# Kernel optimization log

Measured on AMD Instinct MI355X. Metric: run time of the kernel, lower is better.

Reference implementation:

```python
import jax, jax.numpy as jnp
import numpy as np

B, T, DIM = 2, 1024, 1024
H, DH, E, K = 8, 64, 5, 3
SCALE = DH ** -0.5


def topk_mask(scores, k):
    # 0/1 mask of the top-k entries along the last (expert) axis
    _, idx = jax.lax.top_k(scores, k)          # [..., k]
    return jax.nn.one_hot(idx, scores.shape[-1], dtype=scores.dtype).sum(-2)


def setup_inputs() -> dict:
    key = jax.random.key(0)
    ks = jax.random.split(key, 7)
    s = DIM ** -0.5
    x = jax.random.normal(ks[0], (B, T, DIM), jnp.float32)
    Wq = jax.random.normal(ks[1], (DIM, H * DH), jnp.float32) * s
    Wk = jax.random.normal(ks[2], (DIM, H * DH), jnp.float32) * s
    Wv = jax.random.normal(ks[3], (DIM, H * E * DH), jnp.float32) * s
    Ws = jax.random.normal(ks[4], (DIM, H * E), jnp.float32) * s
    Wd = jax.random.normal(ks[5], (DIM, H * E), jnp.float32) * s
    # grouped conv weight: per head h, expert e: map dim_head -> dim
    Wo = jax.random.normal(ks[6], (H, E, DIM, DH), jnp.float32) * (DH ** -0.5)
    causal_mask = jnp.triu(jnp.ones((T, T), bool), 1)[None, None]  # [1,1,T,T]
    return {"x": x, "Wq": Wq, "Wk": Wk, "Wv": Wv, "Ws": Ws, "Wd": Wd,
            "Wo": Wo, "causal_mask": causal_mask}


def reference(x, Wq, Wk, Wv, Ws, Wd, Wo, causal_mask):
    # source-side routing scores (soft: gate values kept on top-k)
    ss = jax.nn.sigmoid((x @ Ws).reshape(B, T, H, E))
    ss = ss * topk_mask(ss, K)
    # destination-side routing (hard 0/1 top-k mask)
    sd = topk_mask(jax.nn.sigmoid((x @ Wd).reshape(B, T, H, E)), K)

    q = (x @ Wq).reshape(B, T, H, DH).transpose(0, 2, 1, 3)  # [B,H,T,DH]
    k = (x @ Wk).reshape(B, T, H, DH).transpose(0, 2, 1, 3)
    v_exp = (x @ Wv).reshape(B, T, H, E, DH)                  # per-expert V
    v = jnp.einsum('bthe,bthed->bhtd', ss, v_exp)             # routed V mix

    scores = jnp.einsum('bhid,bhjd->bhij', q * SCALE, k)
    scores = jnp.where(causal_mask, -1e9, scores)
    probs = jax.nn.softmax(scores, axis=-1)
    o = jnp.einsum('bhij,bhjd->bhid', probs, v)               # [B,H,T,DH]

    # expert output projection (h,e: DH -> DIM), gated by sd, summed over h,e
    out = jnp.einsum('bthe,bhtc,hedc->btd', sd, o, Wo)        # [B,T,DIM]
    return out
```

## Files before the change

### kernel.cpp

```cpp
#include <hip/hip_runtime.h>

typedef unsigned short u16;
typedef __bf16 bf16x8 __attribute__((ext_vector_type(8)));
typedef float floatx4 __attribute__((ext_vector_type(4)));

#define B_   2
#define T_   1024
#define DIM_ 1024
#define H_   8
#define DH_  64
#define E_   5

#define N1   3584
#define M_   2048
#define KOUT 2560

__device__ __forceinline__ u16 f2bf(float f) {
  union { float f; unsigned u; } v; v.f = f;
  unsigned r = v.u + 0x7FFFu + ((v.u >> 16) & 1u);
  return (u16)(r >> 16);
}
__device__ __forceinline__ float bf2f(u16 h) {
  union { unsigned u; float f; } v; v.u = ((unsigned)h) << 16;
  return v.f;
}

__device__ __forceinline__ void async_cp16(const void* g, void* l) {
  __builtin_amdgcn_global_load_lds(
      (const __attribute__((address_space(1))) unsigned int*)g,
      (__attribute__((address_space(3))) unsigned int*)l, 16, 0, 0);
}


__global__ __launch_bounds__(256)
void transpose_all_kernel(const float* __restrict__ Wq, const float* __restrict__ Wk,
                          const float* __restrict__ Wv, u16* __restrict__ WT) {
  __shared__ float tile[32][33];
  int k0 = blockIdx.x * 32;
  int nt = blockIdx.y;
  const float* W; int N, n0, nofs;
  if (nt < 16)      { W = Wq; N = 512;  n0 = nt * 32;        nofs = 0; }
  else if (nt < 32) { W = Wk; N = 512;  n0 = (nt - 16) * 32; nofs = 512; }
  else              { W = Wv; N = 2560; n0 = (nt - 32) * 32; nofs = 1024; }
  int tx = threadIdx.x & 31, ty = threadIdx.x >> 5;
  #pragma unroll
  for (int i = 0; i < 32; i += 8)
    tile[ty + i][tx] = W[(size_t)(k0 + ty + i) * N + n0 + tx];
  __syncthreads();
  #pragma unroll
  for (int i = 0; i < 32; i += 8)
    WT[(size_t)(nofs + n0 + ty + i) * 1024 + k0 + tx] = f2bf(tile[tx][ty + i]);
}

__global__ void build_WoT_kernel(const float* __restrict__ Wo, u16* __restrict__ WoT) {
  int i = blockIdx.x * 256 + threadIdx.x;
  int c4 = i & 15;
  int t  = i >> 4;
  int d  = t / 40;
  int he = t - d * 40;
  float4 v = *(const float4*)(Wo + ((size_t)(he * 1024 + d) * 64 + c4 * 4));
  union { u16 s[4]; uint2 u; } o;
  o.s[0] = f2bf(v.x); o.s[1] = f2bf(v.y); o.s[2] = f2bf(v.z); o.s[3] = f2bf(v.w);
  *(uint2*)(WoT + (size_t)d * KOUT + he * 64 + c4 * 4) = o.u;
}


template <int SPLITK>
__global__ __launch_bounds__(256)
void gemm4w_kernel(const u16* __restrict__ A, const u16* __restrict__ Bm,
                   u16* __restrict__ C, int N, int Kd) {
  constexpr int BK = 32;
  __shared__ __align__(16) u16 As[128 * BK];
  __shared__ __align__(16) u16 Bs[128 * BK];
  const int tid = threadIdx.x;
  const int w = tid >> 6, lane = tid & 63;
  const int ln15 = lane & 15, quad = lane >> 4;
  const int wm = w >> 1, wn = w & 1;
  const int bm0 = blockIdx.x * 128, bn0 = blockIdx.y * 128;
  const int lrow = lane >> 2;
  const int lg8 = (((lane & 3) ^ ((lane >> 3) & 3))) * 8;
  const int swz = (ln15 >> 1) & 3;
  const int kchunk = Kd / SPLITK;
  const int kbeg = blockIdx.z * kchunk;

  floatx4 acc[4][4];
  #pragma unroll
  for (int i = 0; i < 4; ++i)
    #pragma unroll
    for (int j = 0; j < 4; ++j) acc[i][j] = (floatx4){0.f, 0.f, 0.f, 0.f};

  for (int k0 = kbeg; k0 < kbeg + kchunk; k0 += BK) {
    __syncthreads();
    #pragma unroll
    for (int j = 0; j < 2; ++j) {
      int i = w * 2 + j;
      async_cp16(A + (size_t)(bm0 + i * 16 + lrow) * Kd + k0 + lg8, (char*)As + i * 1024);
      async_cp16(Bm + (size_t)(bn0 + i * 16 + lrow) * Kd + k0 + lg8, (char*)Bs + i * 1024);
    }
    __builtin_amdgcn_s_waitcnt(0);
    __syncthreads();

    bf16x8 af[4], bf[4];
    #pragma unroll
    for (int mt = 0; mt < 4; ++mt)
      af[mt] = *(const bf16x8*)(As + (wm * 64 + mt * 16 + ln15) * BK + ((quad ^ swz) * 8));
    #pragma unroll
    for (int nt = 0; nt < 4; ++nt)
      bf[nt] = *(const bf16x8*)(Bs + (wn * 64 + nt * 16 + ln15) * BK + ((quad ^ swz) * 8));
    #pragma unroll
    for (int mt = 0; mt < 4; ++mt)
      #pragma unroll
      for (int nt = 0; nt < 4; ++nt)
        acc[mt][nt] = __builtin_amdgcn_mfma_f32_16x16x32_bf16(af[mt], bf[nt], acc[mt][nt], 0, 0, 0);
  }

  u16* Cz = C + (size_t)blockIdx.z * M_ * N;
  #pragma unroll
  for (int mt = 0; mt < 4; ++mt)
    #pragma unroll
    for (int nt = 0; nt < 4; ++nt)
      #pragma unroll
      for (int r = 0; r < 4; ++r) {
        int m = bm0 + wm * 64 + mt * 16 + quad * 4 + r;
        int n = bn0 + wn * 64 + nt * 16 + ln15;
        Cz[(size_t)m * N + n] = f2bf(acc[mt][nt][r]);
      }
}

__global__ void reduce4_kernel(const u16* __restrict__ Pk, float* __restrict__ out) {
  int i = blockIdx.x * 256 + threadIdx.x;
  size_t base = (size_t)i * 8;
  float s[8] = {0.f, 0.f, 0.f, 0.f, 0.f, 0.f, 0.f, 0.f};
  #pragma unroll
  for (int z = 0; z < 4; ++z) {
    union { uint4 v; u16 h[8]; } u;
    u.v = *(const uint4*)(Pk + (size_t)z * M_ * 1024 + base);
    #pragma unroll
    for (int c = 0; c < 8; ++c) s[c] += bf2f(u.h[c]);
  }
  float4 o0 = {s[0], s[1], s[2], s[3]}, o1 = {s[4], s[5], s[6], s[7]};
  *(float4*)(out + base) = o0;
  *(float4*)(out + base + 4) = o1;
}


__global__ __launch_bounds__(256)
void routing_cvt_kernel(const float* __restrict__ x, const float* __restrict__ Ws,
                        const float* __restrict__ Wd,
                        float* __restrict__ ssg, float* __restrict__ sdg,
                        u16* __restrict__ xb) {
  __shared__ float xs[4][1025];
  __shared__ float ps[3][4][80];
  __shared__ float lg[4][80];
  const int bt0 = blockIdx.x * 4;
  const int tid = threadIdx.x;

  for (int i = tid; i < 1024; i += 256) {
    int r = i >> 8, j = i & 255;
    float4 v = ((const float4*)(x + (size_t)(bt0 + r) * 1024))[j];
    xs[r][j * 4 + 0] = v.x; xs[r][j * 4 + 1] = v.y;
    xs[r][j * 4 + 2] = v.z; xs[r][j * 4 + 3] = v.w;
  }
  __syncthreads();

  for (int i = tid; i < 512; i += 256) {
    int r = i >> 7, j2 = i & 127;
    union { u16 s[8]; uint4 v; } o;
    #pragma unroll
    for (int c = 0; c < 8; ++c) o.s[c] = f2bf(xs[r][j2 * 8 + c]);
    *(uint4*)(xb + (size_t)(bt0 + r) * 1024 + j2 * 8) = o.v;
  }

  const int c = tid % 80, ks = tid / 80;
  if (ks < 3) {
    const float* Wp = (c < 40) ? Ws : Wd;
    const int cc = (c < 40) ? c : c - 40;
    const int k0 = ks * 342, k1 = (k0 + 342 < 1024) ? k0 + 342 : 1024;
    float a0 = 0.f, a1 = 0.f, a2 = 0.f, a3 = 0.f;
    #pragma unroll 4
    for (int k = k0; k < k1; ++k) {
      float wv = Wp[k * 40 + cc];
      a0 = fmaf(xs[0][k], wv, a0); a1 = fmaf(xs[1][k], wv, a1);
      a2 = fmaf(xs[2][k], wv, a2); a3 = fmaf(xs[3][k], wv, a3);
    }
    ps[ks][0][c] = a0; ps[ks][1][c] = a1; ps[ks][2][c] = a2; ps[ks][3][c] = a3;
  }
  __syncthreads();

  for (int idx = tid; idx < 320; idx += 256) {
    int r = idx / 80, cc = idx % 80;
    lg[r][cc] = ps[0][r][cc] + ps[1][r][cc] + ps[2][r][cc];
  }
  __syncthreads();

  if (tid < 64) {
    const int r = tid >> 4, h = (tid >> 1) & 7, which = tid & 1;
    float z[E_], g[E_]; bool sel[E_];
    #pragma unroll
    for (int e = 0; e < E_; ++e) {
      z[e] = lg[r][which * 40 + h * E_ + e];
      g[e] = 1.f / (1.f + __expf(-z[e]));
      sel[e] = false;
    }
    #pragma unroll
    for (int it = 0; it < 3; ++it) {
      int bi = 0; float bv = -3e38f;
      #pragma unroll
      for (int e = 0; e < E_; ++e)
        if (!sel[e] && z[e] > bv) { bv = z[e]; bi = e; }
      sel[bi] = true;
    }
    float* dst = (which == 0) ? ssg : sdg;
    #pragma unroll
    for (int e = 0; e < E_; ++e)
      dst[(size_t)(bt0 + r) * 40 + h * E_ + e] =
          (which == 0) ? (sel[e] ? g[e] : 0.f) : (sel[e] ? 1.f : 0.f);
  }
}


__global__ __launch_bounds__(256)
void vmix_tr_kernel(const u16* __restrict__ c1, const float* __restrict__ ssg,
                    u16* __restrict__ vT) {
  __shared__ u16 tile[32][33];
  const int bh = blockIdx.x;
  const int b = bh >> 3, h = bh & 7;
  const int t0 = blockIdx.y * 32, d0 = blockIdx.z * 32;
  const int dh = threadIdx.x & 31, tl = threadIdx.x >> 5;
  #pragma unroll
  for (int i = 0; i < 4; ++i) {
    int trow = tl + i * 8;
    size_t bt = (size_t)b * T_ + t0 + trow;
    const u16* ve = c1 + bt * N1 + 1024 + h * (E_ * 64) + d0 + dh;
    const float* g = ssg + bt * 40 + h * E_;
    float s = 0.f;
    #pragma unroll
    for (int e = 0; e < E_; ++e) s = fmaf(g[e], bf2f(ve[e * 64]), s);
    tile[trow][dh] = f2bf(s);
  }
  __syncthreads();
  #pragma unroll
  for (int i = 0; i < 4; ++i) {
    int d = d0 + tl + i * 8;
    vT[((size_t)(b * H_ + h) * DH_ + d) * T_ + t0 + dh] = tile[dh][tl + i * 8];
  }
}


__global__ __launch_bounds__(256)
void attn_kernel(const u16* __restrict__ c1, const u16* __restrict__ vT,
                 const float* __restrict__ sdg, u16* __restrict__ Ab) {
  __shared__ __align__(16) u16 Qs[32 * 64];
  __shared__ __align__(16) u16 Ks[2][64 * 64];
  __shared__ __align__(16) u16 Vs[2][64 * 64];
  __shared__ __align__(16) u16 Ps[2][32 * 72];
  __shared__ float Om[2][32][68];
  __shared__ float Ml[2][32], Ll[2][32];
  const int qi = blockIdx.x;
  const int bh = blockIdx.y;
  const int b = bh >> 3, h = bh & 7;
  const int tid = threadIdx.x;
  const int w = tid >> 6, lane = tid & 63;
  const int ln15 = lane & 15, quad = lane >> 4;
  const int hh = w >> 1, wq = w & 1;
  const int q0 = qi * 32;
  const int nkt = (qi >> 1) + 1;
  const int h0n = (nkt + 1) >> 1;
  const int r8 = lane >> 3;
  const int g8 = ((lane & 7) ^ ((lane >> 3) & 7)) * 8;
  const int swz = ln15 & 7;

  async_cp16(c1 + (size_t)(b * T_ + q0 + w * 8 + r8) * N1 + h * DH_ + g8,
             (char*)Qs + w * 1024);

  floatx4 O[4];
  float m_st[4], l_st[4];
  #pragma unroll
  for (int j = 0; j < 4; ++j) {
    O[j] = (floatx4){0.f, 0.f, 0.f, 0.f};
    m_st[j] = -3e38f; l_st[j] = 0.f;
  }
  const int qrow = q0 + wq * 16 + quad * 4;

  for (int j = 0; j < h0n; ++j) {
    const int myt = hh ? (h0n + j) : j;
    const bool act = (hh == 0) || (h0n + j < nkt);
    __syncthreads();
    if (w < 2 || h0n + j < nkt) {
      const int tk = (w < 2 ? j : h0n + j) * 64;
      if ((w & 1) == 0) {
        #pragma unroll
        for (int i = 0; i < 8; ++i)
          async_cp16(c1 + (size_t)(b * T_ + tk + i * 8 + r8) * N1 + 512 + h * DH_ + g8,
                     (char*)Ks[w >> 1] + i * 1024);
      } else {
        #pragma unroll
        for (int i = 0; i < 8; ++i)
          async_cp16(vT + (size_t)((b * H_ + h) * DH_ + i * 8 + r8) * T_ + tk + g8,
                     (char*)Vs[w >> 1] + i * 1024);
      }
    }
    __builtin_amdgcn_s_waitcnt(0);
    __syncthreads();

    float p[4][4];
    if (act) {
      const int tk0 = myt * 64;
      floatx4 S[4];
      #pragma unroll
      for (int nt = 0; nt < 4; ++nt) S[nt] = (floatx4){0.f, 0.f, 0.f, 0.f};
      #pragma unroll
      for (int ks = 0; ks < 2; ++ks) {
        bf16x8 a = *(const bf16x8*)(Qs + (wq * 16 + ln15) * 64 + (((ks * 4 + quad) ^ swz)) * 8);
        #pragma unroll
        for (int nt = 0; nt < 4; ++nt) {
          bf16x8 bv = *(const bf16x8*)(&Ks[hh][(nt * 16 + ln15) * 64 + (((ks * 4 + quad) ^ swz)) * 8]);
          S[nt] = __builtin_amdgcn_mfma_f32_16x16x32_bf16(a, bv, S[nt], 0, 0, 0);
        }
      }
      float rmax[4], alpha[4], rsum[4];
      #pragma unroll
      for (int r = 0; r < 4; ++r) rmax[r] = -3e38f;
      #pragma unroll
      for (int nt = 0; nt < 4; ++nt) {
        int col = tk0 + nt * 16 + ln15;
        #pragma unroll
        for (int r = 0; r < 4; ++r) {
          float s = S[nt][r] * 0.125f;
          if (col > qrow + r) s = -3e38f;
          p[nt][r] = s;
          rmax[r] = fmaxf(rmax[r], s);
        }
      }
      #pragma unroll
      for (int r = 0; r < 4; ++r) {
        #pragma unroll
        for (int off = 1; off < 16; off <<= 1)
          rmax[r] = fmaxf(rmax[r], __shfl_xor(rmax[r], off));
        float mn = fmaxf(m_st[r], rmax[r]);
        alpha[r] = __expf(m_st[r] - mn);
        m_st[r] = mn;
        rsum[r] = 0.f;
      }
      #pragma unroll
      for (int nt = 0; nt < 4; ++nt)
        #pragma unroll
        for (int r = 0; r < 4; ++r) {
          float e = __expf(p[nt][r] - m_st[r]);
          p[nt][r] = e;
          rsum[r] += e;
        }
      #pragma unroll
      for (int r = 0; r < 4; ++r) {
        #pragma unroll
        for (int off = 1; off < 16; off <<= 1)
          rsum[r] += __shfl_xor(rsum[r], off);
        l_st[r] = l_st[r] * alpha[r] + rsum[r];
      }
      #pragma unroll
      for (int nt = 0; nt < 4; ++nt)
        #pragma unroll
        for (int r = 0; r < 4; ++r) O[nt][r] *= alpha[r];
      #pragma unroll
      for (int nt = 0; nt < 4; ++nt)
        #pragma unroll
        for (int r = 0; r < 4; ++r)
          Ps[hh][(wq * 16 + quad * 4 + r) * 72 + nt * 16 + ln15] = f2bf(p[nt][r]);
    }
    __syncthreads();
    if (act) {
      #pragma unroll
      for (int ks = 0; ks < 2; ++ks) {
        bf16x8 a = *(const bf16x8*)(&Ps[hh][(wq * 16 + ln15) * 72 + ks * 32 + quad * 8]);
        #pragma unroll
        for (int nt = 0; nt < 4; ++nt) {
          bf16x8 bv = *(const bf16x8*)(&Vs[hh][(nt * 16 + ln15) * 64 + (((ks * 4 + quad) ^ swz)) * 8]);
          O[nt] = __builtin_amdgcn_mfma_f32_16x16x32_bf16(a, bv, O[nt], 0, 0, 0);
        }
      }
    }
  }

  #pragma unroll
  for (int nt = 0; nt < 4; ++nt)
    #pragma unroll
    for (int r = 0; r < 4; ++r)
      Om[hh][wq * 16 + quad * 4 + r][nt * 16 + ln15] = O[nt][r];
  if (ln15 == 0) {
    #pragma unroll
    for (int r = 0; r < 4; ++r) {
      Ml[hh][wq * 16 + quad * 4 + r] = m_st[r];
      Ll[hh][wq * 16 + quad * 4 + r] = l_st[r];
    }
  }
  __syncthreads();

  const int rr = tid >> 3, cg = (tid & 7) * 8;
  float m0 = Ml[0][rr], m1 = Ml[1][rr];
  float l0 = Ll[0][rr], l1 = Ll[1][rr];
  float m = fmaxf(m0, m1);
  float a0 = __expf(m0 - m), a1 = __expf(m1 - m);
  float inv = 1.f / (l0 * a0 + l1 * a1);
  float oc[8];
  #pragma unroll
  for (int cc = 0; cc < 8; ++cc)
    oc[cc] = (Om[0][rr][cg + cc] * a0 + Om[1][rr][cg + cc] * a1) * inv;
  size_t bt = (size_t)b * T_ + q0 + rr;
  #pragma unroll
  for (int e = 0; e < E_; ++e) {
    float g = sdg[bt * 40 + h * E_ + e];
    union { u16 s[8]; uint4 v; } o;
    #pragma unroll
    for (int cc = 0; cc < 8; ++cc) o.s[cc] = f2bf(g * oc[cc]);
    *(uint4*)(Ab + bt * KOUT + (h * E_ + e) * 64 + cg) = o.v;
  }
}


extern "C" void kernel_launch(void* const* d_in, const int* in_sizes, int n_in,
                              void* d_out, int out_size, void* d_ws, size_t ws_size,
                              hipStream_t stream) {
  const float* x  = (const float*)d_in[0];
  const float* Wq = (const float*)d_in[1];
  const float* Wk = (const float*)d_in[2];
  const float* Wv = (const float*)d_in[3];
  const float* Ws = (const float*)d_in[4];
  const float* Wd = (const float*)d_in[5];
  const float* Wo = (const float*)d_in[6];
  float* out = (float*)d_out;

  char* ws = (char*)d_ws;
  u16*   WoT  = (u16*)(ws + 0);
  u16*   xb   = (u16*)(ws + 5242880);
  u16*   WT   = (u16*)(ws + 9437184);
  u16*   c1   = (u16*)(ws + 16777216);
  float* ssg  = (float*)(ws + 31457280);
  float* sdg  = (float*)(ws + 31784960);
  u16*   vT   = (u16*)(ws + 32112640);
  u16*   Ab   = (u16*)(ws + 34209792);
  u16*   Pk   = (u16*)(ws + 46137344);

  routing_cvt_kernel<<<512, 256, 0, stream>>>(x, Ws, Wd, ssg, sdg, xb);
  transpose_all_kernel<<<dim3(32, 112), 256, 0, stream>>>(Wq, Wk, Wv, WT);
  build_WoT_kernel<<<2560, 256, 0, stream>>>(Wo, WoT);

  gemm4w_kernel<1><<<dim3(16, 28, 1), 256, 0, stream>>>(xb, WT, c1, N1, 1024);

  vmix_tr_kernel<<<dim3(16, 32, 2), 256, 0, stream>>>(c1, ssg, vT);

  attn_kernel<<<dim3(32, 16), 256, 0, stream>>>(c1, vT, sdg, Ab);

  gemm4w_kernel<4><<<dim3(16, 8, 4), 256, 0, stream>>>(Ab, WoT, Pk, 1024, KOUT);
  reduce4_kernel<<<1024, 256, 0, stream>>>(Pk, out);
}
```

Baseline: 208.0 us.

## Split routing into tiled split-K logits GEMM plus separate top-k kernel

Replaces the per-4-row routing kernel, which re-read the full Ws/Wd weights for every 4 tokens with poor parallelism, with a register-tiled 64-row by 80-column split-K logits kernel. That kernel also writes the bf16 copy of x, and a separate top-k kernel then sums the 8 partial logit slabs and applies the sigmoid and top-k selection. The aim is more weight reuse and more active blocks, at the cost of an extra launch and a round trip of partial logits through global memory.

Result: faster. 192.5 us (-7.4%).

```diff
diff --git a/kernel.cpp b/kernel.cpp
--- a/kernel.cpp
+++ b/kernel.cpp
@@ -62,6 +62,107 @@
   union { u16 s[4]; uint2 u; } o;
   o.s[0] = f2bf(v.x); o.s[1] = f2bf(v.y); o.s[2] = f2bf(v.z); o.s[3] = f2bf(v.w);
   *(uint2*)(WoT + (size_t)d * KOUT + he * 64 + c4 * 4) = o.u;
+}
+
+
+__global__ __launch_bounds__(256)
+void logits_kernel(const float* __restrict__ x, const float* __restrict__ Ws,
+                   const float* __restrict__ Wd, float* __restrict__ Pl,
+                   u16* __restrict__ xb) {
+  __shared__ float xs[16][68];
+  __shared__ float wt[16][80];
+  const int tid = threadIdx.x;
+  const int m0 = blockIdx.x * 64;
+  const int kbeg = blockIdx.y * 128;
+  const int tx = tid & 15, ty = tid >> 4;
+  const int srow = tid >> 2, skq = tid & 3;
+
+  float acc[4][5];
+  #pragma unroll
+  for (int r = 0; r < 4; ++r)
+    #pragma unroll
+    for (int c = 0; c < 5; ++c) acc[r][c] = 0.f;
+
+  for (int s = 0; s < 8; ++s) {
+    const int k0 = kbeg + s * 16;
+    __syncthreads();
+    {
+      float4 v = *(const float4*)(x + (size_t)(m0 + srow) * 1024 + k0 + skq * 4);
+      xs[skq * 4 + 0][srow] = v.x; xs[skq * 4 + 1][srow] = v.y;
+      xs[skq * 4 + 2][srow] = v.z; xs[skq * 4 + 3][srow] = v.w;
+      union { u16 h[4]; uint2 u; } o;
+      o.h[0] = f2bf(v.x); o.h[1] = f2bf(v.y); o.h[2] = f2bf(v.z); o.h[3] = f2bf(v.w);
+      *(uint2*)(xb + (size_t)(m0 + srow) * 1024 + k0 + skq * 4) = o.u;
+    }
+    #pragma unroll
+    for (int j = 0; j < 5; ++j) {
+      int f = j * 256 + tid;
+      int kk = f / 80, c = f - kk * 80;
+      wt[kk][c] = (c < 40) ? Ws[(size_t)(k0 + kk) * 40 + c]
+                           : Wd[(size_t)(k0 + kk) * 40 + c - 40];
+    }
+    __syncthreads();
+
+    #pragma unroll
+    for (int kk = 0; kk < 16; ++kk) {
+      float4 xv = *(const float4*)(&xs[kk][ty * 4]);
+      float xr[4] = {xv.x, xv.y, xv.z, xv.w};
+      #pragma unroll
+      for (int c = 0; c < 5; ++c) {
+        float wv = wt[kk][tx * 5 + c];
+        #pragma unroll
+        for (int r = 0; r < 4; ++r) acc[r][c] = fmaf(xr[r], wv, acc[r][c]);
+      }
+    }
+  }
+
+  float* P = Pl + (size_t)blockIdx.y * M_ * 80;
+  #pragma unroll
+  for (int r = 0; r < 4; ++r)
+    #pragma unroll
+    for (int c = 0; c < 5; ++c)
+      P[(size_t)(m0 + ty * 4 + r) * 80 + tx * 5 + c] = acc[r][c];
+}
+
+__global__ __launch_bounds__(256)
+void topk_kernel(const float* __restrict__ Pl, float* __restrict__ ssg,
+                 float* __restrict__ sdg) {
+  __shared__ float lg[16][80];
+  const int bt0 = blockIdx.x * 16;
+  const int tid = threadIdx.x;
+  #pragma unroll
+  for (int j = 0; j < 5; ++j) {
+    int f = j * 256 + tid;
+    int r = f / 80, c = f - r * 80;
+    float s = 0.f;
+    #pragma unroll
+    for (int z = 0; z < 8; ++z)
+      s += Pl[(size_t)z * M_ * 80 + (size_t)(bt0 + r) * 80 + c];
+    lg[r][c] = s;
+  }
+  __syncthreads();
+
+  const int r = tid >> 4, h = (tid >> 1) & 7, side = tid & 1;
+  float z[E_], g[E_]; bool sel[E_];
+  #pragma unroll
+  for (int e = 0; e < E_; ++e) {
+    z[e] = lg[r][side * 40 + h * E_ + e];
+    g[e] = 1.f / (1.f + __expf(-z[e]));
+    sel[e] = false;
+  }
+  #pragma unroll
+  for (int it = 0; it < 3; ++it) {
+    int bi = 0; float bv = -3e38f;
+    #pragma unroll
+    for (int e = 0; e < E_; ++e)
+      if (!sel[e] && z[e] > bv) { bv = z[e]; bi = e; }
+    sel[bi] = true;
+  }
+  float* dst = (side == 0) ? ssg : sdg;
+  #pragma unroll
+  for (int e = 0; e < E_; ++e)
+    dst[(size_t)(bt0 + r) * 40 + h * E_ + e] =
+        (side == 0) ? (sel[e] ? g[e] : 0.f) : (sel[e] ? 1.f : 0.f);
 }
 
 
@@ -141,81 +242,6 @@
   float4 o0 = {s[0], s[1], s[2], s[3]}, o1 = {s[4], s[5], s[6], s[7]};
   *(float4*)(out + base) = o0;
   *(float4*)(out + base + 4) = o1;
-}
-
-
-__global__ __launch_bounds__(256)
-void routing_cvt_kernel(const float* __restrict__ x, const float* __restrict__ Ws,
-                        const float* __restrict__ Wd,
-                        float* __restrict__ ssg, float* __restrict__ sdg,
-                        u16* __restrict__ xb) {
-  __shared__ float xs[4][1025];
-  __shared__ float ps[3][4][80];
-  __shared__ float lg[4][80];
-  const int bt0 = blockIdx.x * 4;
-  const int tid = threadIdx.x;
-
-  for (int i = tid; i < 1024; i += 256) {
-    int r = i >> 8, j = i & 255;
-    float4 v = ((const float4*)(x + (size_t)(bt0 + r) * 1024))[j];
-    xs[r][j * 4 + 0] = v.x; xs[r][j * 4 + 1] = v.y;
-    xs[r][j * 4 + 2] = v.z; xs[r][j * 4 + 3] = v.w;
-  }
-  __syncthreads();
-
-  for (int i = tid; i < 512; i += 256) {
-    int r = i >> 7, j2 = i & 127;
-    union { u16 s[8]; uint4 v; } o;
-    #pragma unroll
-    for (int c = 0; c < 8; ++c) o.s[c] = f2bf(xs[r][j2 * 8 + c]);
-    *(uint4*)(xb + (size_t)(bt0 + r) * 1024 + j2 * 8) = o.v;
-  }
-
-  const int c = tid % 80, ks = tid / 80;
-  if (ks < 3) {
-    const float* Wp = (c < 40) ? Ws : Wd;
-    const int cc = (c < 40) ? c : c - 40;
-    const int k0 = ks * 342, k1 = (k0 + 342 < 1024) ? k0 + 342 : 1024;
-    float a0 = 0.f, a1 = 0.f, a2 = 0.f, a3 = 0.f;
-    #pragma unroll 4
-    for (int k = k0; k < k1; ++k) {
-      float wv = Wp[k * 40 + cc];
-      a0 = fmaf(xs[0][k], wv, a0); a1 = fmaf(xs[1][k], wv, a1);
-      a2 = fmaf(xs[2][k], wv, a2); a3 = fmaf(xs[3][k], wv, a3);
-    }
-    ps[ks][0][c] = a0; ps[ks][1][c] = a1; ps[ks][2][c] = a2; ps[ks][3][c] = a3;
-  }
-  __syncthreads();
-
-  for (int idx = tid; idx < 320; idx += 256) {
-    int r = idx / 80, cc = idx % 80;
-    lg[r][cc] = ps[0][r][cc] + ps[1][r][cc] + ps[2][r][cc];
-  }
-  __syncthreads();
-
-  if (tid < 64) {
-    const int r = tid >> 4, h = (tid >> 1) & 7, which = tid & 1;
-    float z[E_], g[E_]; bool sel[E_];
-    #pragma unroll
-    for (int e = 0; e < E_; ++e) {
-      z[e] = lg[r][which * 40 + h * E_ + e];
-      g[e] = 1.f / (1.f + __expf(-z[e]));
-      sel[e] = false;
-    }
-    #pragma unroll
-    for (int it = 0; it < 3; ++it) {
-      int bi = 0; float bv = -3e38f;
-      #pragma unroll
-      for (int e = 0; e < E_; ++e)
-        if (!sel[e] && z[e] > bv) { bv = z[e]; bi = e; }
-      sel[bi] = true;
-    }
-    float* dst = (which == 0) ? ssg : sdg;
-    #pragma unroll
-    for (int e = 0; e < E_; ++e)
-      dst[(size_t)(bt0 + r) * 40 + h * E_ + e] =
-          (which == 0) ? (sel[e] ? g[e] : 0.f) : (sel[e] ? 1.f : 0.f);
-  }
 }
 
 
@@ -439,8 +465,11 @@
   u16*   vT   = (u16*)(ws + 32112640);
   u16*   Ab   = (u16*)(ws + 34209792);
   u16*   Pk   = (u16*)(ws + 46137344);
-
-  routing_cvt_kernel<<<512, 256, 0, stream>>>(x, Ws, Wd, ssg, sdg, xb);
+  float* Pl   = (float*)(ws + 62914560);
+
+  logits_kernel<<<dim3(32, 8), 256, 0, stream>>>(x, Ws, Wd, Pl, xb);
+  topk_kernel<<<128, 256, 0, stream>>>(Pl, ssg, sdg);
+
   transpose_all_kernel<<<dim3(32, 112), 256, 0, stream>>>(Wq, Wk, Wv, WT);
   build_WoT_kernel<<<2560, 256, 0, stream>>>(Wo, WoT);
 
```
